# Performance work log

Measured on AMD Instinct MI355X. Metric: run time of the kernel, lower is better.

The kernel has to match this reference:

```python
import jax, jax.numpy as jnp
import numpy as np


def setup_inputs() -> dict:
    key = jax.random.key(0)
    x = jax.random.normal(key, (4, 4, 32, 256, 256), dtype=jnp.float32)
    return {"x": x}


def reference(x):
    # NonMaximaSuppression3d with kernel_size=(3,3,3) fast path:
    # a voxel survives iff it is strictly greater than all 26 neighbors;
    # border voxels (no full neighborhood) are always suppressed.
    B, CH, D, H, W = x.shape
    ct = x[..., 1:-1, 1:-1, 1:-1]  # interior centers [B,CH,D-2,H-2,W-2]
    mask_inner = jnp.ones(ct.shape, dtype=bool)
    for dz in range(3):
        for dy in range(3):
            for dx in range(3):
                if (dz, dy, dx) == (1, 1, 1):
                    continue
                neigh = x[..., dz:D - 2 + dz, dy:H - 2 + dy, dx:W - 2 + dx]
                mask_inner = mask_inner & (ct > neigh)
    mask = jnp.zeros(x.shape, dtype=bool).at[..., 1:-1, 1:-1, 1:-1].set(mask_inner)
    return x * mask.astype(x.dtype)
```

## Files before the change

### kernel.cpp

```cpp
#include <hip/hip_runtime.h>


typedef float v4f __attribute__((ext_vector_type(4)));

constexpr int W  = 256;
constexpr int H  = 256;
constexpr int D  = 32;
constexpr int SH = W;
constexpr int SD = W * H;
constexpr int KD = 4;
constexpr int HC = 8;
constexpr int BC = 16;
constexpr int DG = D / KD;
constexpr int HG = H / HC;

__device__ __forceinline__ v4f vmax4(v4f a, v4f b) {
    return (v4f){fmaxf(a.x, b.x), fmaxf(a.y, b.y), fmaxf(a.z, b.z), fmaxf(a.w, b.w)};
}

__global__ __launch_bounds__(256) void nms3d_kernel(const float* __restrict__ x,
                                                    float* __restrict__ out) {
    const int wid  = (blockIdx.x << 2) | (threadIdx.x >> 6);
    const int lane = threadIdx.x & 63;
    const int hc   = wid & (HG - 1);
    const int dg   = (wid >> 5) & (DG - 1);
    const int bc   = wid >> 8;
    const int d0   = dg * KD;
    const int h0   = hc * HC;

    const float* vol  = x   + bc * (D * SD) + (lane << 2);
    float*       ovol = out + bc * (D * SD) + (lane << 2);

    const float* base[KD + 2];
    #pragma unroll
    for (int j = 0; j < KD + 2; ++j) {
        int p = d0 - 1 + j;
        p = p < 0 ? 0 : (p > D - 1 ? D - 1 : p);
        base[j] = vol + p * SD;
    }

    bool dvalid[KD];
    #pragma unroll
    for (int k = 0; k < KD; ++k) {
        const int dd = d0 + k;
        dvalid[k] = (dd > 0) && (dd < D - 1);
    }

    v4f r[KD + 2][3];
    {
        const int hm = (h0 - 1 < 0) ? 0 : h0 - 1;
        #pragma unroll
        for (int j = 0; j < KD + 2; ++j) r[j][0] = *(const v4f*)(base[j] + hm * SH);
        #pragma unroll
        for (int j = 0; j < KD + 2; ++j) r[j][1] = *(const v4f*)(base[j] + h0 * SH);
    }

    #pragma unroll
    for (int i = 0; i < HC; ++i) {
        const int h  = h0 + i;
        const int s0 = i % 3, s1 = (i + 1) % 3, s2 = (i + 2) % 3;

        const int hp = (h + 1 > H - 1) ? H - 1 : h + 1;
        #pragma unroll
        for (int j = 0; j < KD + 2; ++j)
            r[j][s2] = *(const v4f*)(base[j] + hp * SH);

        v4f a2[KD + 2], a3[KD + 2];
        #pragma unroll
        for (int j = 0; j < KD + 2; ++j) {
            a2[j] = vmax4(r[j][s0], r[j][s2]);
            a3[j] = vmax4(a2[j], r[j][s1]);
        }

        const bool hvalid = (h > 0) && (h < H - 1);

        #pragma unroll
        for (int k = 0; k < KD; ++k) {
            v4f v8 = vmax4(vmax4(a3[k], a3[k + 2]), a2[k + 1]);
            const v4f c = r[k + 1][s1];
            float l8 = __shfl_up(v8.w, 1);
            float r8 = __shfl_down(v8.x, 1);
            float lc = __shfl_up(c.w, 1);
            float rc = __shfl_down(c.x, 1);

            float n0 = fmaxf(fmaxf(l8,   v8.x), v8.y);
            float n1 = fmaxf(fmaxf(v8.x, v8.y), v8.z);
            float n2 = fmaxf(fmaxf(v8.y, v8.z), v8.w);
            float n3 = fmaxf(fmaxf(v8.z, v8.w), r8);
            n0 = fmaxf(n0, fmaxf(lc,  c.y));
            n1 = fmaxf(n1, fmaxf(c.x, c.z));
            n2 = fmaxf(n2, fmaxf(c.y, c.w));
            n3 = fmaxf(n3, fmaxf(c.z, rc));

            const bool v = hvalid && dvalid[k];
            v4f o;
            o.x = (v && lane > 0  && c.x > n0) ? c.x : 0.f;
            o.y = (v && c.y > n1) ? c.y : 0.f;
            o.z = (v && c.z > n2) ? c.z : 0.f;
            o.w = (v && lane < 63 && c.w > n3) ? c.w : 0.f;
            __builtin_nontemporal_store(o, (v4f*)(ovol + (d0 + k) * SD + h * SH));
        }
    }
}

extern "C" void kernel_launch(void* const* d_in, const int* in_sizes, int n_in,
                              void* d_out, int out_size, void* d_ws, size_t ws_size,
                              hipStream_t stream) {
    const float* x = (const float*)d_in[0];
    float* out = (float*)d_out;
    const int grid = (BC * DG * HG) / 4;
    nms3d_kernel<<<grid, 256, 0, stream>>>(x, out);
}
```

Before: 237.0 us.

## Stage block tile in LDS via global_load_lds, one depth plane per wave

Each block now loads a (KD+2)x(HC+2) row tile into shared memory using direct global-to-LDS loads, then each of the four waves computes one depth plane from LDS. This cuts per-wave register pressure and lets the four waves share the halo rows rather than each loading its own. In exchange it uses about 60 KB of LDS per block, which limits blocks per CU, and it adds a block-wide barrier with no overlap between loading and computing.

```diff
diff --git a/kernel.cpp b/kernel.cpp
--- a/kernel.cpp
+++ b/kernel.cpp
@@ -13,6 +13,9 @@
 constexpr int BC = 16;
 constexpr int DG = D / KD;
 constexpr int HG = H / HC;
+constexpr int NPL = KD + 2;
+constexpr int NR  = HC + 2;
+constexpr int TROWS = NPL * NR;
 
 __device__ __forceinline__ v4f vmax4(v4f a, v4f b) {
     return (v4f){fmaxf(a.x, b.x), fmaxf(a.y, b.y), fmaxf(a.z, b.z), fmaxf(a.w, b.w)};
@@ -20,86 +23,82 @@
 
 __global__ __launch_bounds__(256) void nms3d_kernel(const float* __restrict__ x,
                                                     float* __restrict__ out) {
-    const int wid  = (blockIdx.x << 2) | (threadIdx.x >> 6);
+    __shared__ float lds[TROWS * W];
+
+    const int blk  = blockIdx.x;
+    const int wv   = threadIdx.x >> 6;
     const int lane = threadIdx.x & 63;
-    const int hc   = wid & (HG - 1);
-    const int dg   = (wid >> 5) & (DG - 1);
-    const int bc   = wid >> 8;
+    const int hc   = blk & (HG - 1);
+    const int dg   = (blk >> 5) & (DG - 1);
+    const int bc   = blk >> 8;
     const int d0   = dg * KD;
     const int h0   = hc * HC;
 
-    const float* vol  = x   + bc * (D * SD) + (lane << 2);
-    float*       ovol = out + bc * (D * SD) + (lane << 2);
+    const float* vol = x + bc * (D * SD);
 
-    const float* base[KD + 2];
     #pragma unroll
-    for (int j = 0; j < KD + 2; ++j) {
-        int p = d0 - 1 + j;
-        p = p < 0 ? 0 : (p > D - 1 ? D - 1 : p);
-        base[j] = vol + p * SD;
+    for (int u = 0; u < TROWS / 4; ++u) {
+        const int t = wv * (TROWS / 4) + u;
+        const int j = t / NR;
+        const int r = t - j * NR;
+        int p = d0 - 1 + j;  p = p < 0 ? 0 : (p > D - 1 ? D - 1 : p);
+        int hh = h0 - 1 + r; hh = hh < 0 ? 0 : (hh > H - 1 ? H - 1 : hh);
+        const float* gp = vol + p * SD + hh * SH + (lane << 2);
+        __builtin_amdgcn_global_load_lds(
+            (const __attribute__((address_space(1))) unsigned int*)gp,
+            (__attribute__((address_space(3))) unsigned int*)&lds[(j * NR + r) * W],
+            16, 0, 0);
     }
+    __syncthreads();
 
-    bool dvalid[KD];
-    #pragma unroll
-    for (int k = 0; k < KD; ++k) {
-        const int dd = d0 + k;
-        dvalid[k] = (dd > 0) && (dd < D - 1);
-    }
+    const int d = d0 + wv;
+    const bool dv = (d > 0) && (d < D - 1);
+    float* ovol = out + bc * (D * SD) + d * SD + (lane << 2);
 
-    v4f r[KD + 2][3];
-    {
-        const int hm = (h0 - 1 < 0) ? 0 : h0 - 1;
-        #pragma unroll
-        for (int j = 0; j < KD + 2; ++j) r[j][0] = *(const v4f*)(base[j] + hm * SH);
-        #pragma unroll
-        for (int j = 0; j < KD + 2; ++j) r[j][1] = *(const v4f*)(base[j] + h0 * SH);
-    }
+    const float* Lm = lds + (wv * NR) * W + (lane << 2);
+    const float* L0 = lds + ((wv + 1) * NR) * W + (lane << 2);
+    const float* Lp = lds + ((wv + 2) * NR) * W + (lane << 2);
+
+    v4f rm[3], r0[3], rp[3];
+    rm[0] = *(const v4f*)(Lm + 0 * W); r0[0] = *(const v4f*)(L0 + 0 * W); rp[0] = *(const v4f*)(Lp + 0 * W);
+    rm[1] = *(const v4f*)(Lm + 1 * W); r0[1] = *(const v4f*)(L0 + 1 * W); rp[1] = *(const v4f*)(Lp + 1 * W);
 
     #pragma unroll
     for (int i = 0; i < HC; ++i) {
-        const int h  = h0 + i;
         const int s0 = i % 3, s1 = (i + 1) % 3, s2 = (i + 2) % 3;
+        rm[s2] = *(const v4f*)(Lm + (i + 2) * W);
+        r0[s2] = *(const v4f*)(L0 + (i + 2) * W);
+        rp[s2] = *(const v4f*)(Lp + (i + 2) * W);
 
-        const int hp = (h + 1 > H - 1) ? H - 1 : h + 1;
-        #pragma unroll
-        for (int j = 0; j < KD + 2; ++j)
-            r[j][s2] = *(const v4f*)(base[j] + hp * SH);
+        const v4f a3m = vmax4(vmax4(rm[s0], rm[s1]), rm[s2]);
+        const v4f a3p = vmax4(vmax4(rp[s0], rp[s1]), rp[s2]);
+        const v4f a20 = vmax4(r0[s0], r0[s2]);
+        const v4f v8  = vmax4(vmax4(a3m, a3p), a20);
+        const v4f c   = r0[s1];
 
-        v4f a2[KD + 2], a3[KD + 2];
-        #pragma unroll
-        for (int j = 0; j < KD + 2; ++j) {
-            a2[j] = vmax4(r[j][s0], r[j][s2]);
-            a3[j] = vmax4(a2[j], r[j][s1]);
-        }
+        const float l8 = __shfl_up(v8.w, 1);
+        const float r8 = __shfl_down(v8.x, 1);
+        const float lc = __shfl_up(c.w, 1);
+        const float rc = __shfl_down(c.x, 1);
 
-        const bool hvalid = (h > 0) && (h < H - 1);
+        float n0 = fmaxf(fmaxf(l8,   v8.x), v8.y);
+        float n1 = fmaxf(fmaxf(v8.x, v8.y), v8.z);
+        float n2 = fmaxf(fmaxf(v8.y, v8.z), v8.w);
+        float n3 = fmaxf(fmaxf(v8.z, v8.w), r8);
+        n0 = fmaxf(n0, fmaxf(lc,  c.y));
+        n1 = fmaxf(n1, fmaxf(c.x, c.z));
+        n2 = fmaxf(n2, fmaxf(c.y, c.w));
+        n3 = fmaxf(n3, fmaxf(c.z, rc));
 
-        #pragma unroll
-        for (int k = 0; k < KD; ++k) {
-            v4f v8 = vmax4(vmax4(a3[k], a3[k + 2]), a2[k + 1]);
-            const v4f c = r[k + 1][s1];
-            float l8 = __shfl_up(v8.w, 1);
-            float r8 = __shfl_down(v8.x, 1);
-            float lc = __shfl_up(c.w, 1);
-            float rc = __shfl_down(c.x, 1);
-
-            float n0 = fmaxf(fmaxf(l8,   v8.x), v8.y);
-            float n1 = fmaxf(fmaxf(v8.x, v8.y), v8.z);
-            float n2 = fmaxf(fmaxf(v8.y, v8.z), v8.w);
-            float n3 = fmaxf(fmaxf(v8.z, v8.w), r8);
-            n0 = fmaxf(n0, fmaxf(lc,  c.y));
-            n1 = fmaxf(n1, fmaxf(c.x, c.z));
-            n2 = fmaxf(n2, fmaxf(c.y, c.w));
-            n3 = fmaxf(n3, fmaxf(c.z, rc));
-
-            const bool v = hvalid && dvalid[k];
-            v4f o;
-            o.x = (v && lane > 0  && c.x > n0) ? c.x : 0.f;
-            o.y = (v && c.y > n1) ? c.y : 0.f;
-            o.z = (v && c.z > n2) ? c.z : 0.f;
-            o.w = (v && lane < 63 && c.w > n3) ? c.w : 0.f;
-            __builtin_nontemporal_store(o, (v4f*)(ovol + (d0 + k) * SD + h * SH));
-        }
+        const int h = h0 + i;
+        const bool hv = (h > 0) && (h < H - 1);
+        const bool v  = hv && dv;
+        v4f o;
+        o.x = (v && lane > 0  && c.x > n0) ? c.x : 0.f;
+        o.y = (v && c.y > n1) ? c.y : 0.f;
+        o.z = (v && c.z > n2) ? c.z : 0.f;
+        o.w = (v && lane < 63 && c.w > n3) ? c.w : 0.f;
+        __builtin_nontemporal_store(o, (v4f*)(ovol + h * SH));
     }
 }
 
@@ -108,6 +107,6 @@
                               hipStream_t stream) {
     const float* x = (const float*)d_in[0];
     float* out = (float*)d_out;
-    const int grid = (BC * DG * HG) / 4;
+    const int grid = BC * DG * HG;
     nms3d_kernel<<<grid, 256, 0, stream>>>(x, out);
 }
```

New measurement: 223.3 us. 1.06x faster.
